# Kernel optimization log

Hardware: AMD Instinct MI355X
Metric: run time of the kernel (lower is better)

## Reference

```python
import jax, jax.numpy as jnp
import numpy as np

B, T, C, H = 4, 2048, 1024, 16
D = C // H  # head_dim = 64


def setup_inputs() -> dict:
    key = jax.random.key(0)
    k1, k2, k3, k4 = jax.random.split(key, 4)
    x = jax.random.normal(k1, (B, T, C), dtype=jnp.float32)
    # realistic padding: each sequence has length in [T//2, T]
    lengths = jax.random.randint(k4, (B,), T // 2, T + 1)
    padding_mask = jnp.arange(T)[None, :] < lengths[:, None]  # True = keep
    # weights stored [in, out] (equivalent to torch Linear weight transposed)
    w_qkv = jax.random.normal(k2, (C, 3 * C), dtype=jnp.float32) * (C ** -0.5)
    w_out = jax.random.normal(k3, (C, C), dtype=jnp.float32) * (C ** -0.5)
    b_out = jnp.zeros((C,), dtype=jnp.float32)
    return {"x": x, "padding_mask": padding_mask, "w_qkv": w_qkv, "w_out": w_out, "b_out": b_out}


def reference(x, padding_mask, w_qkv, w_out, b_out):
    scale = D ** -0.5
    qkv = x @ w_qkv  # [B,T,3C]
    q, k, v = jnp.split(qkv, 3, axis=-1)

    def split_heads(t):
        return t.reshape(B, T, H, D).transpose(0, 2, 1, 3)  # [B,H,T,D]

    q, k, v = split_heads(q), split_heads(k), split_heads(v)
    attn = jnp.einsum("bhqd,bhkd->bhqk", q, k) * scale  # [B,H,T,T]
    mask = padding_mask[:, None, None, :]  # [B,1,1,T]
    attn = jnp.where(mask, attn, jnp.finfo(attn.dtype).min)
    attn = jax.nn.softmax(attn, axis=-1)
    # dropout is identity in eval mode
    out = jnp.einsum("bhqk,bhkd->bhqd", attn, v)  # [B,H,T,D]
    out = out.transpose(0, 2, 1, 3).reshape(B, T, C)
    return out @ w_out + b_out
```

## Files before the change

kernel.cpp:

```cpp
#include <hip/hip_runtime.h>
#include <hip/hip_bf16.h>

#define Bb 4
#define Tt 2048
#define Cc 1024
#define Hh 16

typedef unsigned short u16;
typedef __attribute__((ext_vector_type(8))) __bf16 bf16x8;
typedef __attribute__((ext_vector_type(4))) float  f32x4;

__device__ __forceinline__ u16 f2bf_hw(float f) {
    __bf16 h = (__bf16)f;
    return *(u16*)&h;
}

__device__ __forceinline__ float fexp2(float x) {
#if __has_builtin(__builtin_amdgcn_exp2f)
    return __builtin_amdgcn_exp2f(x);
#else
    return __expf(x * 0.6931471805599453f);
#endif
}

__device__ __forceinline__ void gld_lds16(const void* g, void* l) {
    __builtin_amdgcn_global_load_lds(
        (__attribute__((address_space(1))) void*)(g),
        (__attribute__((address_space(3))) void*)(l),
        16, 0, 0);
}

__device__ __forceinline__ f32x4 mfma16(bf16x8 a, bf16x8 b, f32x4 c) {
    return __builtin_amdgcn_mfma_f32_16x16x32_bf16(a, b, c, 0, 0, 0);
}

__global__ void cast_f32_bf16(const float* __restrict__ in, u16* __restrict__ out, int n4) {
    int i = blockIdx.x * 256 + threadIdx.x;
    if (i < n4) {
        float4 v = ((const float4*)in)[i];
        uint2 o;
        o.x = (unsigned)f2bf_hw(v.x) | ((unsigned)f2bf_hw(v.y) << 16);
        o.y = (unsigned)f2bf_hw(v.z) | ((unsigned)f2bf_hw(v.w) << 16);
        ((uint2*)out)[i] = o;
    }
}

__global__ void castT_f32_bf16(const float* __restrict__ in, u16* __restrict__ out,
                               int K, int N) {
    __shared__ float Ls[64][65];
    const int n0 = blockIdx.x * 64, k0 = blockIdx.y * 64;
    const int t = threadIdx.x;
    #pragma unroll
    for (int s = 0; s < 4; ++s) {
        int idx = t + 256 * s;
        int r   = idx >> 4;
        int c4  = (idx & 15) * 4;
        float4 v = *(const float4*)&in[(size_t)(k0 + r) * N + n0 + c4];
        Ls[r][c4 + 0] = v.x; Ls[r][c4 + 1] = v.y;
        Ls[r][c4 + 2] = v.z; Ls[r][c4 + 3] = v.w;
    }
    __syncthreads();
    #pragma unroll
    for (int s = 0; s < 2; ++s) {
        int idx = t + 256 * s;
        int n   = idx >> 3;
        int kc  = (idx & 7) * 8;
        alignas(16) u16 tmp[8];
        #pragma unroll
        for (int i = 0; i < 8; ++i) tmp[i] = f2bf_hw(Ls[kc + i][n]);
        *(uint4*)&out[(size_t)(n0 + n) * K + k0 + kc] = *(const uint4*)tmp;
    }
}

__global__ void repack_vT(const u16* __restrict__ qkv, u16* __restrict__ vT) {
    const int t = threadIdx.x, w = t >> 6, lane = t & 63;
    const int tile = blockIdx.x, bh = blockIdx.y, b = bh >> 4, h = bh & 15;
    #pragma unroll
    for (int u = 0; u < 2; ++u) {
        int tc = tile * 64 + (2 * w + u) * 8;
        alignas(16) u16 tmp[8];
        #pragma unroll
        for (int i = 0; i < 8; ++i)
            tmp[i] = qkv[(size_t)(b * Tt + tc + i) * (3 * Cc) + 2 * Cc + h * 64 + lane];
        *(uint4*)&vT[((size_t)(bh * 64) + lane) * Tt + tc] = *(const uint4*)tmp;
    }
}

__global__ __launch_bounds__(256, 3) void gemm_bt_bf16(
    const u16* __restrict__ A, const u16* __restrict__ Bt,
    const float* __restrict__ bias,
    u16* __restrict__ outB, float* __restrict__ outF,
    int M, int N, int K)
{
    __shared__ u16 As[128 * 32];
    __shared__ u16 Bs[128 * 32];
    const int t = threadIdx.x;
    const int w = t >> 6, lane = t & 63;
    const int quad = lane >> 4, l16 = lane & 15;
    const int wr = w >> 1, wc = w & 1;
    const int m0 = blockIdx.y * 128, n0 = blockIdx.x * 128;

    int aoff[4], boff[4];
    #pragma unroll
    for (int i = 0; i < 4; ++i) {
        int rA = 64 * wr + 16 * i + l16;
        aoff[i] = rA * 32 + ((quad ^ ((rA >> 1) & 3)) * 8);
        int rB = 64 * wc + 16 * i + l16;
        boff[i] = rB * 32 + ((quad ^ ((rB >> 1) & 3)) * 8);
    }

    f32x4 acc[4][4] = {};

    for (int k0 = 0; k0 < K; k0 += 32) {
        __syncthreads();
        #pragma unroll
        for (int u = 0; u < 2; ++u) {
            const int i   = 2 * w + u;
            const int row = 16 * i + (lane >> 2);
            const int c   = (lane & 3) ^ ((row >> 1) & 3);
            gld_lds16(A  + (size_t)(m0 + row) * K + k0 + c * 8, (void*)(As + i * 512 + lane * 8));
            gld_lds16(Bt + (size_t)(n0 + row) * K + k0 + c * 8, (void*)(Bs + i * 512 + lane * 8));
        }
        asm volatile("s_waitcnt vmcnt(0)" ::: "memory");
        __syncthreads();

        bf16x8 af[4], bfr[4];
        #pragma unroll
        for (int i = 0; i < 4; ++i) af[i]  = *(const bf16x8*)&As[aoff[i]];
        #pragma unroll
        for (int j = 0; j < 4; ++j) bfr[j] = *(const bf16x8*)&Bs[boff[j]];
        #pragma unroll
        for (int i = 0; i < 4; ++i)
            #pragma unroll
            for (int j = 0; j < 4; ++j)
                acc[i][j] = mfma16(af[i], bfr[j], acc[i][j]);
    }

    const int rbase = m0 + 64 * wr + quad * 4;
    const int cbase = n0 + 64 * wc + l16;
    if (outF) {
        float bv[4];
        #pragma unroll
        for (int j = 0; j < 4; ++j) bv[j] = bias[cbase + 16 * j];
        #pragma unroll
        for (int i = 0; i < 4; ++i)
            #pragma unroll
            for (int r = 0; r < 4; ++r) {
                size_t ro = (size_t)(rbase + 16 * i + r) * N;
                #pragma unroll
                for (int j = 0; j < 4; ++j)
                    outF[ro + cbase + 16 * j] = acc[i][j][r] + bv[j];
            }
    } else {
        #pragma unroll
        for (int i = 0; i < 4; ++i)
            #pragma unroll
            for (int r = 0; r < 4; ++r) {
                size_t ro = (size_t)(rbase + 16 * i + r) * N;
                #pragma unroll
                for (int j = 0; j < 4; ++j)
                    outB[ro + cbase + 16 * j] = f2bf_hw(acc[i][j][r]);
            }
    }
}

__global__ __launch_bounds__(256, 2) void attn_mfma(
    const u16* __restrict__ qkv, const u16* __restrict__ vT,
    const int* __restrict__ mask, u16* __restrict__ outO)
{
    __shared__ u16 Qs[128 * 64];
    __shared__ u16 Ks[2][64 * 64];
    __shared__ u16 Vs[2][64 * 64];
    __shared__ u16 Ps[128 * 72];
    __shared__ int Lsh;

    const int t = threadIdx.x, w = t >> 6, lane = t & 63;
    const int quad = lane >> 4, l16 = lane & 15;
    const int qt = blockIdx.x, bh = blockIdx.y, b = bh >> 4, h = bh & 15;

    if (t == 0) Lsh = 0;
    __syncthreads();
    int partial = 0;
    #pragma unroll
    for (int k = 0; k < Tt / 256; ++k) partial += mask[b * Tt + t + 256 * k];
    #pragma unroll
    for (int off = 32; off > 0; off >>= 1) partial += __shfl_down(partial, off);
    if (lane == 0) atomicAdd(&Lsh, partial);

    const size_t kbase = (size_t)(b * Tt) * (3 * Cc) + Cc + h * 64;
    const size_t vbase = (size_t)(bh * 64) * Tt;
    const int srow = lane >> 3, scol = lane & 7;

    auto stage = [&](int ch, int buf) {
        const int kc = ch * 64;
        #pragma unroll
        for (int u = 0; u < 2; ++u) {
            const int i = 2 * w + u;
            const int row = 8 * i + srow;
            const int c = scol ^ (row & 7);
            gld_lds16(qkv + kbase + (size_t)(kc + row) * (3 * Cc) + c * 8,
                      (void*)(Ks[buf] + i * 512 + lane * 8));
            gld_lds16(vT + vbase + (size_t)row * Tt + kc + c * 8,
                      (void*)(Vs[buf] + i * 512 + lane * 8));
        }
    };

    const size_t qbase = (size_t)(b * Tt + qt * 128) * (3 * Cc) + h * 64;
    #pragma unroll
    for (int u = 0; u < 4; ++u) {
        const int i = 4 * w + u;
        const int row = 8 * i + srow;
        const int c = scol ^ (row & 7);
        gld_lds16(qkv + qbase + (size_t)row * (3 * Cc) + c * 8, (void*)(Qs + i * 512 + lane * 8));
    }
    stage(0, 0);
    asm volatile("s_waitcnt vmcnt(0)" ::: "memory");
    __syncthreads();
    const int L = Lsh;

    bf16x8 qf[2][2];
    #pragma unroll
    for (int qq = 0; qq < 2; ++qq) {
        const int rq = 32 * w + 16 * qq + l16;
        #pragma unroll
        for (int ks = 0; ks < 2; ++ks)
            qf[qq][ks] = *(const bf16x8*)&Qs[rq * 64 + (((quad + 4 * ks) ^ (rq & 7)) * 8)];
    }
    int koff[4][2];
    #pragma unroll
    for (int i = 0; i < 4; ++i) {
        int r = 16 * i + l16;
        #pragma unroll
        for (int ks = 0; ks < 2; ++ks)
            koff[i][ks] = r * 64 + (((quad + 4 * ks) ^ (r & 7)) * 8);
    }
    const int prow = 32 * w + l16;

    f32x4 oacc[2][4] = {};
    float lsum[2] = {};
    const float c2 = 0.18033688011112042f;

    const int nfull = L >> 6;
    const int nch   = (L + 63) >> 6;

    for (int ch = 0; ch < nch; ++ch) {
        if (ch + 1 < nch) stage(ch + 1, (ch + 1) & 1);
        const u16* ks_ = Ks[ch & 1];
        const u16* vs_ = Vs[ch & 1];

        bf16x8 kf[4][2], vf[4][2];
        #pragma unroll
        for (int i = 0; i < 4; ++i)
            #pragma unroll
            for (int ks = 0; ks < 2; ++ks) {
                kf[i][ks] = *(const bf16x8*)&ks_[koff[i][ks]];
                vf[i][ks] = *(const bf16x8*)&vs_[koff[i][ks]];
            }

        #pragma unroll
        for (int qq = 0; qq < 2; ++qq) {
            f32x4 st[4];
            #pragma unroll
            for (int jt = 0; jt < 4; ++jt) {
                f32x4 z = {0.f, 0.f, 0.f, 0.f};
                z = mfma16(kf[jt][0], qf[qq][0], z);
                st[jt] = mfma16(kf[jt][1], qf[qq][1], z);
            }
            if (ch < nfull) {
                #pragma unroll
                for (int jt = 0; jt < 4; ++jt) {
                    float e0 = fexp2(st[jt][0] * c2);
                    float e1 = fexp2(st[jt][1] * c2);
                    float e2 = fexp2(st[jt][2] * c2);
                    float e3 = fexp2(st[jt][3] * c2);
                    lsum[qq] += (e0 + e1) + (e2 + e3);
                    uint2 pk;
                    pk.x = (unsigned)f2bf_hw(e0) | ((unsigned)f2bf_hw(e1) << 16);
                    pk.y = (unsigned)f2bf_hw(e2) | ((unsigned)f2bf_hw(e3) << 16);
                    *(uint2*)&Ps[(prow + 16 * qq) * 72 + 16 * jt + quad * 4] = pk;
                }
            } else {
                const int kc = ch * 64;
                #pragma unroll
                for (int jt = 0; jt < 4; ++jt) {
                    const int kb = kc + 16 * jt + quad * 4;
                    float e[4];
                    #pragma unroll
                    for (int r = 0; r < 4; ++r) {
                        e[r] = (kb + r < L) ? fexp2(st[jt][r] * c2) : 0.f;
                        lsum[qq] += e[r];
                    }
                    uint2 pk;
                    pk.x = (unsigned)f2bf_hw(e[0]) | ((unsigned)f2bf_hw(e[1]) << 16);
                    pk.y = (unsigned)f2bf_hw(e[2]) | ((unsigned)f2bf_hw(e[3]) << 16);
                    *(uint2*)&Ps[(prow + 16 * qq) * 72 + 16 * jt + quad * 4] = pk;
                }
            }
        }

        #pragma unroll
        for (int qq = 0; qq < 2; ++qq)
            #pragma unroll
            for (int ks = 0; ks < 2; ++ks) {
                bf16x8 pf = *(const bf16x8*)&Ps[(prow + 16 * qq) * 72 + quad * 8 + 32 * ks];
                #pragma unroll
                for (int dt = 0; dt < 4; ++dt)
                    oacc[qq][dt] = mfma16(pf, vf[dt][ks], oacc[qq][dt]);
            }

        asm volatile("s_waitcnt vmcnt(0)" ::: "memory");
        __syncthreads();
    }

    #pragma unroll
    for (int qq = 0; qq < 2; ++qq) {
        float v = lsum[qq];
        v += __shfl_xor(v, 16);
        v += __shfl_xor(v, 32);
        lsum[qq] = v;
    }

    const int orow0 = qt * 128 + 32 * w;
    #pragma unroll
    for (int qq = 0; qq < 2; ++qq)
        #pragma unroll
        for (int r = 0; r < 4; ++r) {
            const float inv = 1.f / __shfl(lsum[qq], quad * 4 + r);
            const size_t ro = (size_t)(b * Tt + orow0 + 16 * qq + quad * 4 + r) * Cc + h * 64;
            #pragma unroll
            for (int dt = 0; dt < 4; ++dt)
                outO[ro + 16 * dt + l16] = f2bf_hw(oacc[qq][dt][r] * inv);
        }
}

extern "C" void kernel_launch(void* const* d_in, const int* in_sizes, int n_in,
                              void* d_out, int out_size, void* d_ws, size_t ws_size,
                              hipStream_t stream) {
    const float* x     = (const float*)d_in[0];
    const int*   mask  = (const int*)  d_in[1];
    const float* w_qkv = (const float*)d_in[2];
    const float* w_out = (const float*)d_in[3];
    const float* b_out = (const float*)d_in[4];
    float*       outp  = (float*)d_out;

    const int M = Bb * Tt;
    char* ws = (char*)d_ws;
    u16* xb     = (u16*)(ws);
    u16* wqkvT  = (u16*)(ws + (16u << 20));
    u16* woutT  = (u16*)(ws + (22u << 20));
    u16* qkv    = (u16*)(ws + (24u << 20));
    u16* vT     = (u16*)(ws + (72u << 20));
    u16* attnO  = (u16*)(ws + (88u << 20));

    cast_f32_bf16<<<(M * Cc / 4 + 255) / 256, 256, 0, stream>>>(x, xb, M * Cc / 4);
    castT_f32_bf16<<<dim3(3 * Cc / 64, Cc / 64), 256, 0, stream>>>(w_qkv, wqkvT, Cc, 3 * Cc);
    castT_f32_bf16<<<dim3(Cc / 64, Cc / 64), 256, 0, stream>>>(w_out, woutT, Cc, Cc);

    gemm_bt_bf16<<<dim3(3 * Cc / 128, M / 128), 256, 0, stream>>>(
        xb, wqkvT, nullptr, qkv, nullptr, M, 3 * Cc, Cc);

    repack_vT<<<dim3(Tt / 64, Bb * Hh), 256, 0, stream>>>(qkv, vT);

    attn_mfma<<<dim3(Tt / 128, Bb * Hh), 256, 0, stream>>>(qkv, vT, mask, attnO);

    gemm_bt_bf16<<<dim3(Cc / 128, M / 128), 256, 0, stream>>>(
        attnO, woutT, b_out, nullptr, outp, M, Cc, Cc);
}
```

Baseline: 279.0 us.

## Restructure attention into single-wave blocks loading K/V directly from global memory

Result: slower. 305.9 us (+9.7%).

```diff
diff --git a/kernel.cpp b/kernel.cpp
--- a/kernel.cpp
+++ b/kernel.cpp
@@ -164,101 +164,63 @@
     }
 }
 
-__global__ __launch_bounds__(256, 2) void attn_mfma(
+__global__ __launch_bounds__(64, 2) void attn_mfma(
     const u16* __restrict__ qkv, const u16* __restrict__ vT,
     const int* __restrict__ mask, u16* __restrict__ outO)
 {
-    __shared__ u16 Qs[128 * 64];
-    __shared__ u16 Ks[2][64 * 64];
-    __shared__ u16 Vs[2][64 * 64];
-    __shared__ u16 Ps[128 * 72];
-    __shared__ int Lsh;
-
-    const int t = threadIdx.x, w = t >> 6, lane = t & 63;
+    __shared__ u16 Ps[64 * 72];
+
+    const int lane = threadIdx.x;
     const int quad = lane >> 4, l16 = lane & 15;
     const int qt = blockIdx.x, bh = blockIdx.y, b = bh >> 4, h = bh & 15;
 
-    if (t == 0) Lsh = 0;
-    __syncthreads();
-    int partial = 0;
-    #pragma unroll
-    for (int k = 0; k < Tt / 256; ++k) partial += mask[b * Tt + t + 256 * k];
-    #pragma unroll
-    for (int off = 32; off > 0; off >>= 1) partial += __shfl_down(partial, off);
-    if (lane == 0) atomicAdd(&Lsh, partial);
-
-    const size_t kbase = (size_t)(b * Tt) * (3 * Cc) + Cc + h * 64;
-    const size_t vbase = (size_t)(bh * 64) * Tt;
-    const int srow = lane >> 3, scol = lane & 7;
-
-    auto stage = [&](int ch, int buf) {
-        const int kc = ch * 64;
-        #pragma unroll
-        for (int u = 0; u < 2; ++u) {
-            const int i = 2 * w + u;
-            const int row = 8 * i + srow;
-            const int c = scol ^ (row & 7);
-            gld_lds16(qkv + kbase + (size_t)(kc + row) * (3 * Cc) + c * 8,
-                      (void*)(Ks[buf] + i * 512 + lane * 8));
-            gld_lds16(vT + vbase + (size_t)row * Tt + kc + c * 8,
-                      (void*)(Vs[buf] + i * 512 + lane * 8));
-        }
-    };
-
-    const size_t qbase = (size_t)(b * Tt + qt * 128) * (3 * Cc) + h * 64;
-    #pragma unroll
-    for (int u = 0; u < 4; ++u) {
-        const int i = 4 * w + u;
-        const int row = 8 * i + srow;
-        const int c = scol ^ (row & 7);
-        gld_lds16(qkv + qbase + (size_t)row * (3 * Cc) + c * 8, (void*)(Qs + i * 512 + lane * 8));
-    }
-    stage(0, 0);
-    asm volatile("s_waitcnt vmcnt(0)" ::: "memory");
-    __syncthreads();
-    const int L = Lsh;
-
-    bf16x8 qf[2][2];
-    #pragma unroll
-    for (int qq = 0; qq < 2; ++qq) {
-        const int rq = 32 * w + 16 * qq + l16;
-        #pragma unroll
-        for (int ks = 0; ks < 2; ++ks)
-            qf[qq][ks] = *(const bf16x8*)&Qs[rq * 64 + (((quad + 4 * ks) ^ (rq & 7)) * 8)];
-    }
-    int koff[4][2];
-    #pragma unroll
-    for (int i = 0; i < 4; ++i) {
-        int r = 16 * i + l16;
-        #pragma unroll
-        for (int ks = 0; ks < 2; ++ks)
-            koff[i][ks] = r * 64 + (((quad + 4 * ks) ^ (r & 7)) * 8);
-    }
-    const int prow = 32 * w + l16;
-
-    f32x4 oacc[2][4] = {};
-    float lsum[2] = {};
+    int sum = 0;
+    {
+        const int4* mp = (const int4*)(mask + b * Tt) + lane * 8;
+        #pragma unroll
+        for (int i = 0; i < 8; ++i) { int4 m4 = mp[i]; sum += m4.x + m4.y + m4.z + m4.w; }
+        #pragma unroll
+        for (int off = 1; off < 64; off <<= 1) sum += __shfl_xor(sum, off);
+    }
+    const int L = sum;
+
+    const int q0 = qt * 64;
+    bf16x8 qf[4][2];
+    #pragma unroll
+    for (int qq = 0; qq < 4; ++qq) {
+        const u16* qp = qkv + (size_t)(b * Tt + q0 + 16 * qq + l16) * (3 * Cc) + h * 64 + quad * 8;
+        qf[qq][0] = *(const bf16x8*)(qp);
+        qf[qq][1] = *(const bf16x8*)(qp + 32);
+    }
+
+    const u16* kp0 = qkv + (size_t)(b * Tt) * (3 * Cc) + Cc + h * 64 + quad * 8;
+    const u16* vp0 = vT + (size_t)(bh * 64) * Tt + quad * 8;
+
+    f32x4 oacc[4][4] = {};
+    f32x4 lacc[4]    = {};
+    const __bf16 onebf = (__bf16)1.0f;
+    const bf16x8 ones  = {onebf, onebf, onebf, onebf, onebf, onebf, onebf, onebf};
     const float c2 = 0.18033688011112042f;
 
     const int nfull = L >> 6;
     const int nch   = (L + 63) >> 6;
 
     for (int ch = 0; ch < nch; ++ch) {
-        if (ch + 1 < nch) stage(ch + 1, (ch + 1) & 1);
-        const u16* ks_ = Ks[ch & 1];
-        const u16* vs_ = Vs[ch & 1];
+        const int kc = ch * 64;
 
         bf16x8 kf[4][2], vf[4][2];
         #pragma unroll
-        for (int i = 0; i < 4; ++i)
-            #pragma unroll
-            for (int ks = 0; ks < 2; ++ks) {
-                kf[i][ks] = *(const bf16x8*)&ks_[koff[i][ks]];
-                vf[i][ks] = *(const bf16x8*)&vs_[koff[i][ks]];
-            }
-
-        #pragma unroll
-        for (int qq = 0; qq < 2; ++qq) {
+        for (int jt = 0; jt < 4; ++jt) {
+            const u16* kp = kp0 + (size_t)(kc + 16 * jt + l16) * (3 * Cc);
+            kf[jt][0] = *(const bf16x8*)(kp);
+            kf[jt][1] = *(const bf16x8*)(kp + 32);
+            const u16* vp = vp0 + (size_t)(16 * jt + l16) * Tt + kc;
+            vf[jt][0] = *(const bf16x8*)(vp);
+            vf[jt][1] = *(const bf16x8*)(vp + 32);
+        }
+
+        #pragma unroll
+        for (int qq = 0; qq < 4; ++qq) {
             f32x4 st[4];
             #pragma unroll
             for (int jt = 0; jt < 4; ++jt) {
@@ -266,6 +228,7 @@
                 z = mfma16(kf[jt][0], qf[qq][0], z);
                 st[jt] = mfma16(kf[jt][1], qf[qq][1], z);
             }
+            uint2 pk[4];
             if (ch < nfull) {
                 #pragma unroll
                 for (int jt = 0; jt < 4; ++jt) {
@@ -273,63 +236,45 @@
                     float e1 = fexp2(st[jt][1] * c2);
                     float e2 = fexp2(st[jt][2] * c2);
                     float e3 = fexp2(st[jt][3] * c2);
-                    lsum[qq] += (e0 + e1) + (e2 + e3);
-                    uint2 pk;
-                    pk.x = (unsigned)f2bf_hw(e0) | ((unsigned)f2bf_hw(e1) << 16);
-                    pk.y = (unsigned)f2bf_hw(e2) | ((unsigned)f2bf_hw(e3) << 16);
-                    *(uint2*)&Ps[(prow + 16 * qq) * 72 + 16 * jt + quad * 4] = pk;
+                    pk[jt].x = (unsigned)f2bf_hw(e0) | ((unsigned)f2bf_hw(e1) << 16);
+                    pk[jt].y = (unsigned)f2bf_hw(e2) | ((unsigned)f2bf_hw(e3) << 16);
                 }
             } else {
-                const int kc = ch * 64;
                 #pragma unroll
                 for (int jt = 0; jt < 4; ++jt) {
                     const int kb = kc + 16 * jt + quad * 4;
                     float e[4];
                     #pragma unroll
-                    for (int r = 0; r < 4; ++r) {
+                    for (int r = 0; r < 4; ++r)
                         e[r] = (kb + r < L) ? fexp2(st[jt][r] * c2) : 0.f;
-                        lsum[qq] += e[r];
-                    }
-                    uint2 pk;
-                    pk.x = (unsigned)f2bf_hw(e[0]) | ((unsigned)f2bf_hw(e[1]) << 16);
-                    pk.y = (unsigned)f2bf_hw(e[2]) | ((unsigned)f2bf_hw(e[3]) << 16);
-                    *(uint2*)&Ps[(prow + 16 * qq) * 72 + 16 * jt + quad * 4] = pk;
+                    pk[jt].x = (unsigned)f2bf_hw(e[0]) | ((unsigned)f2bf_hw(e[1]) << 16);
+                    pk[jt].y = (unsigned)f2bf_hw(e[2]) | ((unsigned)f2bf_hw(e[3]) << 16);
                 }
             }
-        }
-
-        #pragma unroll
-        for (int qq = 0; qq < 2; ++qq)
+            #pragma unroll
+            for (int jt = 0; jt < 4; ++jt)
+                *(uint2*)&Ps[(16 * qq + l16) * 72 + 16 * jt + quad * 4] = pk[jt];
+
             #pragma unroll
             for (int ks = 0; ks < 2; ++ks) {
-                bf16x8 pf = *(const bf16x8*)&Ps[(prow + 16 * qq) * 72 + quad * 8 + 32 * ks];
+                bf16x8 pf = *(const bf16x8*)&Ps[(16 * qq + l16) * 72 + 32 * ks + quad * 8];
                 #pragma unroll
                 for (int dt = 0; dt < 4; ++dt)
                     oacc[qq][dt] = mfma16(pf, vf[dt][ks], oacc[qq][dt]);
-            }
-
-        asm volatile("s_waitcnt vmcnt(0)" ::: "memory");
-        __syncthreads();
-    }
-
-    #pragma unroll
-    for (int qq = 0; qq < 2; ++qq) {
-        float v = lsum[qq];
-        v += __shfl_xor(v, 16);
-        v += __shfl_xor(v, 32);
-        lsum[qq] = v;
-    }
-
-    const int orow0 = qt * 128 + 32 * w;
-    #pragma unroll
-    for (int qq = 0; qq < 2; ++qq)
+                lacc[qq] = mfma16(pf, ones, lacc[qq]);
+            }
+        }
+    }
+
+    #pragma unroll
+    for (int qq = 0; qq < 4; ++qq)
         #pragma unroll
         for (int r = 0; r < 4; ++r) {
-            const float inv = 1.f / __shfl(lsum[qq], quad * 4 + r);
-            const size_t ro = (size_t)(b * Tt + orow0 + 16 * qq + quad * 4 + r) * Cc + h * 64;
+            const float inv = 1.f / lacc[qq][r];
+            const size_t ro = (size_t)(b * Tt + q0 + 16 * qq + quad * 4 + r) * Cc + h * 64 + l16;
             #pragma unroll
             for (int dt = 0; dt < 4; ++dt)
-                outO[ro + 16 * dt + l16] = f2bf_hw(oacc[qq][dt][r] * inv);
+                outO[ro + 16 * dt] = f2bf_hw(oacc[qq][dt][r] * inv);
         }
 }
 
@@ -361,7 +306,7 @@
 
     repack_vT<<<dim3(Tt / 64, Bb * Hh), 256, 0, stream>>>(qkv, vT);
 
-    attn_mfma<<<dim3(Tt / 128, Bb * Hh), 256, 0, stream>>>(qkv, vT, mask, attnO);
+    attn_mfma<<<dim3(Tt / 64, Bb * Hh), 64, 0, stream>>>(qkv, vT, mask, attnO);
 
     gemm_bt_bf16<<<dim3(Cc / 128, M / 128), 256, 0, stream>>>(
         attnO, woutT, b_out, nullptr, outp, M, Cc, Cc);
```
